# Kernel tuning notes

Measured on AMD Instinct MI355X. Metric: run time of the kernel, lower is better.

Reference implementation:

```python
import jax, jax.numpy as jnp
import numpy as np

B, T, D_MODEL = 2, 2048, 2048
H, HD = 16, 128          # num_heads, head_dim
KV_L, Q_L, R = 512, 1024, 64  # kv_latent, q_latent, qk_rope_dim


def apply_rope(x, freqs):
    # x: (..., T, R); freqs: (T, R//2) angles theta (torch stores exp(i*theta))
    # torch pairs consecutive elements: view(..., R//2, 2) as complex
    xr = x.reshape(x.shape[:-1] + (R // 2, 2))
    x0, x1 = xr[..., 0], xr[..., 1]
    cos, sin = jnp.cos(freqs), jnp.sin(freqs)  # broadcast over leading dims
    y0 = x0 * cos - x1 * sin
    y1 = x0 * sin + x1 * cos
    return jnp.stack([y0, y1], axis=-1).reshape(x.shape)


def setup_inputs() -> dict:
    key = jax.random.key(0)
    ks = jax.random.split(key, 10)
    s = 0.02
    return {
        "x": jax.random.normal(ks[0], (B, T, D_MODEL), jnp.float32),
        "freqs": jax.random.normal(ks[1], (T, R // 2), jnp.float32),
        # weights stored as (in, out) so forward is x @ W (== torch x @ W.T)
        "W_DKV": jax.random.normal(ks[2], (D_MODEL, KV_L), jnp.float32) * s,
        "W_UK": jax.random.normal(ks[3], (KV_L, H * HD), jnp.float32) * s,
        "W_UV": jax.random.normal(ks[4], (KV_L, H * HD), jnp.float32) * s,
        "W_KR": jax.random.normal(ks[5], (D_MODEL, R), jnp.float32) * s,
        "W_DQ": jax.random.normal(ks[6], (D_MODEL, Q_L), jnp.float32) * s,
        "W_UQ": jax.random.normal(ks[7], (Q_L, H * HD), jnp.float32) * s,
        "W_QR": jax.random.normal(ks[8], (Q_L, H * R), jnp.float32) * s,
        "W_O": jax.random.normal(ks[9], (H * HD, D_MODEL), jnp.float32) * s,
    }


def reference(x, freqs, W_DKV, W_UK, W_UV, W_KR, W_DQ, W_UQ, W_QR, W_O):
    b, t, _ = x.shape
    # compressed KV latent and expansions
    c_KV = x @ W_DKV                                             # (B,T,KV_L)
    K_c = (c_KV @ W_UK).reshape(b, t, H, HD).transpose(0, 2, 1, 3)  # (B,H,T,HD)
    V = (c_KV @ W_UV).reshape(b, t, H, HD).transpose(0, 2, 1, 3)    # (B,H,T,HD)
    # shared (single-head) rope key
    K_r1 = apply_rope((x @ W_KR)[:, None, :, :], freqs)          # (B,1,T,R)
    K_r = jnp.broadcast_to(K_r1, (b, H, t, R))
    # compressed Q latent
    c_Q = x @ W_DQ                                               # (B,T,Q_L)
    Q_c = (c_Q @ W_UQ).reshape(b, t, H, HD).transpose(0, 2, 1, 3)
    Q_r = apply_rope((c_Q @ W_QR).reshape(b, t, H, R).transpose(0, 2, 1, 3), freqs)
    Q = jnp.concatenate([Q_c, Q_r], axis=-1)                     # (B,H,T,HD+R)
    K = jnp.concatenate([K_c, K_r], axis=-1)
    # causal SDPA, scale = 1/sqrt(HD+R) (torch default: query last dim)
    scale = 1.0 / jnp.sqrt(jnp.asarray(HD + R, Q.dtype))
    scores = jnp.einsum("bhqe,bhke->bhqk", Q, K) * scale
    causal = jnp.tril(jnp.ones((t, t), bool))
    scores = jnp.where(causal, scores, jnp.asarray(-1e30, scores.dtype))
    attn = jax.nn.softmax(scores, axis=-1)
    out = jnp.einsum("bhqk,bhkd->bhqd", attn, V)                 # (B,H,T,HD)
    out = out.transpose(0, 2, 1, 3).reshape(b, t, H * HD)
    y = out @ W_O                                                # (B,T,D_MODEL)
    return (y, c_KV, K_r1[:, 0, :, :])
```

## Files before the change

### kernel.cpp

```cpp
#include <hip/hip_runtime.h>
#include <stdint.h>

typedef unsigned short u16;
typedef __attribute__((ext_vector_type(8))) short s16x8;
typedef __attribute__((ext_vector_type(4))) float f32x4;

#define B_   2
#define T_   2048
#define DM   2048
#define H_   16
#define HD_  128
#define R_   64
#define E_   192
#define SCALE2 0.104117542f

__device__ __forceinline__ u16 f2b(float f) {
  union { float f; uint32_t u; } x; x.f = f;
  uint32_t u = x.u;
  return (u16)((u + 0x7FFFu + ((u >> 16) & 1u)) >> 16);
}
__device__ __forceinline__ float b2f(u16 h) {
  union { uint32_t u; float f; } x; x.u = ((uint32_t)h) << 16;
  return x.f;
}
__device__ __forceinline__ unsigned pk2(float a, float b) {
  union { float f; unsigned u; } A, B; A.f = a; B.f = b;
  return (B.u & 0xFFFF0000u) | (A.u >> 16);
}
__device__ __forceinline__ void ld_lds16(const void* g, void* l) {
  __builtin_amdgcn_global_load_lds((const __attribute__((address_space(1))) void*)g,
                                   (__attribute__((address_space(3))) void*)l,
                                   16, 0, 0);
}

__device__ __forceinline__ void conv_dev(const float* __restrict__ in, u16* __restrict__ out, int i) {
  float4 v = *(const float4*)(in + (size_t)i * 4);
  ushort4 o;
  o.x = f2b(v.x); o.y = f2b(v.y); o.z = f2b(v.z); o.w = f2b(v.w);
  *(ushort4*)(out + (size_t)i * 4) = o;
}
__device__ __forceinline__ void tr64(const float* __restrict__ in, u16* __restrict__ out,
                                     int K, int N, int bx, int by) {
  __shared__ u16 t[64][65];
  int bn = bx * 64, bk = by * 64;
  int tid = threadIdx.x;
  int r0 = tid >> 4, c0 = (tid & 15) * 4;
#pragma unroll
  for (int rr = 0; rr < 64; rr += 16) {
    float4 v = *(const float4*)(in + (size_t)(bk + r0 + rr) * N + bn + c0);
    t[r0 + rr][c0 + 0] = f2b(v.x); t[r0 + rr][c0 + 1] = f2b(v.y);
    t[r0 + rr][c0 + 2] = f2b(v.z); t[r0 + rr][c0 + 3] = f2b(v.w);
  }
  __syncthreads();
#pragma unroll
  for (int rr = 0; rr < 64; rr += 16) {
    ushort4 v;
    v.x = t[c0 + 0][r0 + rr]; v.y = t[c0 + 1][r0 + rr];
    v.z = t[c0 + 2][r0 + rr]; v.w = t[c0 + 3][r0 + rr];
    *(ushort4*)(out + (size_t)(bn + r0 + rr) * K + bk + c0) = v;
  }
}

__global__ __launch_bounds__(256)
void ta_k(const float* __restrict__ x, const float* __restrict__ fr,
          u16* __restrict__ x_bf, u16* __restrict__ fr_bf,
          const float* __restrict__ wdkv, const float* __restrict__ wkr,
          const float* __restrict__ wdq, u16* __restrict__ W) {
  int id = blockIdx.x;
  if (id < 8192)        conv_dev(x, x_bf, id * 256 + threadIdx.x);
  else if (id < 8256)   conv_dev(fr, fr_bf, (id - 8192) * 256 + threadIdx.x);
  else if (id < 8512) { int i = id - 8256; tr64(wdkv, W, 2048, 512, i & 7, i >> 3); }
  else if (id < 8544) { int i = id - 8512; tr64(wkr, W + 512 * 2048, 2048, 64, 0, i); }
  else                { int i = id - 8544; tr64(wdq, W + 576 * 2048, 2048, 1024, i & 15, i >> 4); }
}
__global__ __launch_bounds__(256)
void tb1_k(const float* __restrict__ wuk, const float* __restrict__ wuv, u16* __restrict__ W) {
  int id = blockIdx.x;
  if (id < 256) tr64(wuk, W, 512, 2048, id & 31, id >> 5);
  else { int i = id - 256; tr64(wuv, W + 2048 * 512, 512, 2048, i & 31, i >> 5); }
}
__global__ __launch_bounds__(256)
void tb2_k(const float* __restrict__ wuq, const float* __restrict__ wqr, u16* __restrict__ W) {
  int id = blockIdx.x;
  if (id < 512) tr64(wuq, W, 1024, 2048, id & 31, id >> 5);
  else { int i = id - 512; tr64(wqr, W + 2048 * 1024, 1024, 1024, i & 15, i >> 4); }
}
__global__ __launch_bounds__(256)
void tc_k(const float* __restrict__ wo, u16* __restrict__ W) {
  tr64(wo, W, 2048, 2048, blockIdx.x & 31, blockIdx.x >> 5);
}

template <int EPI>
__global__ __launch_bounds__(256)
void gemm_bf16(const u16* __restrict__ A, const u16* __restrict__ Bt,
               u16* __restrict__ O0, u16* __restrict__ O1, u16* __restrict__ O2,
               float* __restrict__ OF, float* __restrict__ OF2,
               const u16* __restrict__ FR, int M, int N, int K) {
  __shared__ __align__(16) u16 Al[2][128 * 32];
  __shared__ __align__(16) u16 Bl[2][128 * 32];
  const int tid = threadIdx.x;
  const int ln = tid & 63, w = tid >> 6;
  const int quad = ln >> 4, l16 = ln & 15;
  const int wm = (w >> 1) * 64, wn = (w & 1) * 64;
  const int m0 = blockIdx.y * 128, n0 = blockIdx.x * 128;

  f32x4 zz = {0.f, 0.f, 0.f, 0.f};
  f32x4 acc[4][4];
#pragma unroll
  for (int i = 0; i < 4; i++)
#pragma unroll
    for (int j = 0; j < 4; j++) acc[i][j] = zz;

  const u16* aG[2];
  const u16* bG[2];
  int ldsC[2];
#pragma unroll
  for (int r = 0; r < 2; r++) {
    int i = tid + r * 256;
    int row = i >> 2, cq = (i & 3) * 8;
    aG[r] = A + (size_t)(m0 + row) * K + cq;
    int rb = n0 + row;
    if (rb > N - 1) rb = N - 1;
    bG[r] = Bt + (size_t)rb * K + cq;
    ldsC[r] = ((tid & ~63) + r * 256) * 8;
  }

  for (int k = 0; k < K; k += 64) {
#pragma unroll
    for (int hh = 0; hh < 2; hh++)
#pragma unroll
      for (int r = 0; r < 2; r++) {
        ld_lds16(aG[r] + k + hh * 32, &Al[hh][ldsC[r]]);
        ld_lds16(bG[r] + k + hh * 32, &Bl[hh][ldsC[r]]);
      }
    __syncthreads();
#pragma unroll
    for (int hh = 0; hh < 2; hh++) {
      s16x8 af[4], bf[4];
#pragma unroll
      for (int f = 0; f < 4; f++)
        af[f] = *(const s16x8*)&Al[hh][(wm + f * 16 + l16) * 32 + quad * 8];
#pragma unroll
      for (int f = 0; f < 4; f++)
        bf[f] = *(const s16x8*)&Bl[hh][(wn + f * 16 + l16) * 32 + quad * 8];
#pragma unroll
      for (int i = 0; i < 4; i++)
#pragma unroll
        for (int j = 0; j < 4; j++)
          acc[i][j] = __builtin_amdgcn_mfma_f32_16x16x32_bf16(af[i], bf[j], acc[i][j], 0, 0, 0);
    }
    __syncthreads();
  }

#pragma unroll
  for (int fm = 0; fm < 4; fm++) {
#pragma unroll
    for (int fn = 0; fn < 4; fn++) {
      int n = n0 + wn + fn * 16 + l16;
      int mb = m0 + wm + fm * 16 + quad * 4;
      if (EPI == 2) {
        if (n < N) {
#pragma unroll
          for (int rg = 0; rg < 4; rg++) OF[(size_t)(mb + rg) * N + n] = acc[fm][fn][rg];
        }
      } else if (EPI == 4) {
        if (n < 2048) {
#pragma unroll
          for (int rg = 0; rg < 4; rg++) O0[(size_t)(mb + rg) * 2048 + n] = f2b(acc[fm][fn][rg]);
        } else {
          int hd = n - 2048, b = mb >> 11, t = mb & 2047;
          ushort4 v;
          v.x = f2b(acc[fm][fn][0]); v.y = f2b(acc[fm][fn][1]);
          v.z = f2b(acc[fm][fn][2]); v.w = f2b(acc[fm][fn][3]);
          *(ushort4*)(O1 + ((size_t)(b * 2048 + hd) * 2048 + t)) = v;
        }
      } else if (EPI == 5) {
        if (n < 2048) {
#pragma unroll
          for (int rg = 0; rg < 4; rg++) O0[(size_t)(mb + rg) * 2048 + n] = f2b(acc[fm][fn][rg]);
        } else {
#pragma unroll
          for (int rg = 0; rg < 4; rg++) O1[(size_t)(mb + rg) * 1024 + (n - 2048)] = f2b(acc[fm][fn][rg]);
        }
      } else {
        if (n < 512) {
#pragma unroll
          for (int rg = 0; rg < 4; rg++) {
            float v = acc[fm][fn][rg];
            O0[(size_t)(mb + rg) * 512 + n] = f2b(v);
            OF[(size_t)(mb + rg) * 512 + n] = v;
          }
        } else if (n < 576) {
          int r = n - 512, r2 = r >> 1, odd = r & 1;
#pragma unroll
          for (int rg = 0; rg < 4; rg++) {
            float v = acc[fm][fn][rg];
            float p = __shfl_xor(v, 1);
            int t = mb + rg;
            float a = b2f(FR[(size_t)(t & 2047) * 32 + r2]);
            float sn, cs;
            __sincosf(a, &sn, &cs);
            float y = odd ? (p * sn + v * cs) : (v * cs - p * sn);
            O1[(size_t)t * 64 + r] = f2b(y);
            OF2[(size_t)t * 64 + r] = y;
          }
        } else if (n < 1600) {
#pragma unroll
          for (int rg = 0; rg < 4; rg++) O2[(size_t)(mb + rg) * 1024 + (n - 576)] = f2b(acc[fm][fn][rg]);
        }
      }
    }
  }
}

#define KT_S 200
#define VT_S 72
__global__ __launch_bounds__(512, 2)
void flash_attn(const u16* __restrict__ Qc, const u16* __restrict__ Qr,
                const u16* __restrict__ Kc, const u16* __restrict__ Kr,
                const u16* __restrict__ VT, const u16* __restrict__ fr,
                u16* __restrict__ O) {
  __shared__ __align__(16) u16 Kt[64 * KT_S];
  __shared__ __align__(16) u16 Vt[144 * VT_S];

  const int tid = threadIdx.x;
  const int ln = tid & 63, w = tid >> 6;
  const int quad = ln >> 4, l16 = ln & 15;
  const int bh = blockIdx.x, b = bh >> 4, h = bh & 15;

  for (int i = tid; i < 1024; i += 512) Vt[(128 + (i >> 6)) * VT_S + (i & 63)] = 0x3F80;

  const u16* kBase[3]; int kStep[3], kLds[3];
#pragma unroll
  for (int r = 0; r < 3; r++) {
    int i = tid + r * 512;
    int key = i / 24, c = i - key * 24;
    kLds[r] = key * KT_S + c * 8;
    if (c < 16) { kBase[r] = Kc + ((size_t)(b * T_ + key) * DM + h * HD_ + c * 8); kStep[r] = 64 * DM; }
    else        { kBase[r] = Kr + ((size_t)(b * T_ + key) * R_ + (c - 16) * 8);    kStep[r] = 64 * R_; }
  }
  const u16* vBase[2]; int vLds[2];
#pragma unroll
  for (int r = 0; r < 2; r++) {
    int i = tid + r * 512;
    int row = i >> 3, c = i & 7, c2 = c & 3;
    vLds[r] = row * VT_S + (c >> 2) * 32 + ((2 * c2) & 3) * 8 + (c2 >> 1) * 4;
    vBase[r] = VT + ((size_t)(bh * HD_ + row) * T_ + c * 8);
  }

  f32x4 zz = {0.f, 0.f, 0.f, 0.f};
  const int q0 = (15 - (int)blockIdx.y) * 128;
  const int qw = q0 + w * 16;

  s16x8 qf[6];
  {
    int t = qw + l16;
    const u16* p = Qc + ((size_t)(b * T_ + t) * DM + h * HD_ + quad * 8);
#pragma unroll
    for (int f = 0; f < 4; f++) qf[f] = *(const s16x8*)(p + f * 32);
    const u16* pr = Qr + ((size_t)(b * T_ + t) * (H_ * R_) + h * R_ + quad * 8);
#pragma unroll
    for (int half = 0; half < 2; half++) {
      s16x8 v = *(const s16x8*)(pr + half * 32);
      s16x8 o2;
#pragma unroll
      for (int p2 = 0; p2 < 4; p2++) {
        float a = b2f(fr[t * 32 + half * 16 + quad * 4 + p2]);
        float sn, cs;
        __sincosf(a, &sn, &cs);
        float x0 = b2f((u16)v[2 * p2]), x1 = b2f((u16)v[2 * p2 + 1]);
        o2[2 * p2] = (short)f2b(x0 * cs - x1 * sn);
        o2[2 * p2 + 1] = (short)f2b(x0 * sn + x1 * cs);
      }
      qf[4 + half] = o2;
    }
  }

  f32x4 o[9];
#pragma unroll
  for (int f = 0; f < 9; f++) o[f] = zz;
  float mL = -1e30f;

  const u16* pk[3]; const u16* pv[2];
  s16x8 kv[3], vv[2];
#pragma unroll
  for (int r = 0; r < 3; r++) { pk[r] = kBase[r]; kv[r] = *(const s16x8*)pk[r]; }
#pragma unroll
  for (int r = 0; r < 2; r++) { pv[r] = vBase[r]; vv[r] = *(const s16x8*)pv[r]; }

  const int nk = q0 + 128;
  for (int k0 = 0; k0 < nk; k0 += 64) {
    __syncthreads();
#pragma unroll
    for (int r = 0; r < 3; r++) *(s16x8*)&Kt[kLds[r]] = kv[r];
#pragma unroll
    for (int r = 0; r < 2; r++) {
      union { s16x8 v; uint4 u; } V_; V_.v = vv[r];
      uint2 lo; lo.x = V_.u.x; lo.y = V_.u.y;
      uint2 hi; hi.x = V_.u.z; hi.y = V_.u.w;
      *(uint2*)&Vt[vLds[r]] = lo;
      *(uint2*)&Vt[vLds[r] + 8] = hi;
    }
    __syncthreads();
    if (k0 + 64 < nk) {
#pragma unroll
      for (int r = 0; r < 3; r++) { pk[r] += kStep[r]; kv[r] = *(const s16x8*)pk[r]; }
#pragma unroll
      for (int r = 0; r < 2; r++) { pv[r] += 64; vv[r] = *(const s16x8*)pv[r]; }
    }
    if (k0 > qw + 15) continue;

    f32x4 s[4];
#pragma unroll
    for (int kg = 0; kg < 4; kg++) s[kg] = zz;
#pragma unroll
    for (int e = 0; e < 6; e++)
#pragma unroll
      for (int kg = 0; kg < 4; kg++) {
        s16x8 kf = *(const s16x8*)&Kt[(kg * 16 + l16) * KT_S + e * 32 + quad * 8];
        s[kg] = __builtin_amdgcn_mfma_f32_16x16x32_bf16(kf, qf[e], s[kg], 0, 0, 0);
      }
    const int q = qw + l16;
    float sv[16];
    if (k0 + 63 <= qw) {
#pragma unroll
      for (int kg = 0; kg < 4; kg++)
#pragma unroll
        for (int rg = 0; rg < 4; rg++) sv[kg * 4 + rg] = s[kg][rg] * SCALE2;
    } else {
#pragma unroll
      for (int kg = 0; kg < 4; kg++)
#pragma unroll
        for (int rg = 0; rg < 4; rg++) {
          int key = k0 + kg * 16 + quad * 4 + rg;
          sv[kg * 4 + rg] = (key > q) ? -1e30f : s[kg][rg] * SCALE2;
        }
    }
    float mxa = fmaxf(fmaxf(sv[0], sv[1]), fmaxf(sv[2], sv[3]));
    float mxb = fmaxf(fmaxf(sv[4], sv[5]), fmaxf(sv[6], sv[7]));
    float mxc = fmaxf(fmaxf(sv[8], sv[9]), fmaxf(sv[10], sv[11]));
    float mxd = fmaxf(fmaxf(sv[12], sv[13]), fmaxf(sv[14], sv[15]));
    float mx = fmaxf(fmaxf(mxa, mxb), fmaxf(mxc, mxd));
    mx = fmaxf(mx, __shfl_xor(mx, 16));
    mx = fmaxf(mx, __shfl_xor(mx, 32));
    if (__any(mx > mL)) {
      float mn = fmaxf(mL, mx);
      float alpha = exp2f(mL - mn);
      mL = mn;
      float al[4];
#pragma unroll
      for (int rg = 0; rg < 4; rg++) al[rg] = __shfl(alpha, (ln & 48) | (quad * 4 + rg));
#pragma unroll
      for (int f = 0; f < 9; f++)
#pragma unroll
        for (int rg = 0; rg < 4; rg++) o[f][rg] *= al[rg];
    }
    float p[16];
#pragma unroll
    for (int j = 0; j < 16; j++) p[j] = exp2f(sv[j] - mL);
    union { unsigned pw[8]; s16x8 pa[2]; } P_;
#pragma unroll
    for (int kg = 0; kg < 4; kg++) {
      P_.pw[kg * 2 + 0] = pk2(p[kg * 4 + 0], p[kg * 4 + 1]);
      P_.pw[kg * 2 + 1] = pk2(p[kg * 4 + 2], p[kg * 4 + 3]);
    }
#pragma unroll
    for (int f = 0; f < 9; f++) {
      s16x8 vb0 = *(const s16x8*)&Vt[(f * 16 + l16) * VT_S + quad * 8];
      o[f] = __builtin_amdgcn_mfma_f32_16x16x32_bf16(P_.pa[0], vb0, o[f], 0, 0, 0);
      s16x8 vb1 = *(const s16x8*)&Vt[(f * 16 + l16) * VT_S + 32 + quad * 8];
      o[f] = __builtin_amdgcn_mfma_f32_16x16x32_bf16(P_.pa[1], vb1, o[f], 0, 0, 0);
    }
  }

  float inv[4];
#pragma unroll
  for (int rg = 0; rg < 4; rg++) inv[rg] = 1.0f / o[8][rg];
#pragma unroll
  for (int f = 0; f < 8; f++) {
#pragma unroll
    for (int rg = 0; rg < 4; rg++) {
      int qq = qw + quad * 4 + rg;
      O[(size_t)(b * T_ + qq) * DM + h * HD_ + f * 16 + l16] = f2b(o[f][rg] * inv[rg]);
    }
  }
}

extern "C" void kernel_launch(void* const* d_in, const int* in_sizes, int n_in,
                              void* d_out, int out_size, void* d_ws, size_t ws_size,
                              hipStream_t stream) {
  const float* x    = (const float*)d_in[0];
  const float* fr   = (const float*)d_in[1];
  const float* wdkv = (const float*)d_in[2];
  const float* wuk  = (const float*)d_in[3];
  const float* wuv  = (const float*)d_in[4];
  const float* wkr  = (const float*)d_in[5];
  const float* wdq  = (const float*)d_in[6];
  const float* wuq  = (const float*)d_in[7];
  const float* wqr  = (const float*)d_in[8];
  const float* wo   = (const float*)d_in[9];
  u16* ws = (u16*)d_ws;

  const int M1 = 1048576;
  u16* x_bf  = ws;
  u16* Om    = ws;
  u16* Kc    = ws + 8 * M1;
  u16* VTm   = ws + 16 * M1;
  u16* Qc    = ws + 24 * M1;
  u16* Qr    = ws + 32 * M1;
  u16* W     = ws + 36 * M1;
  u16* cKV   = ws + 40 * M1;
  u16* cQ    = ws + 42 * M1;
  u16* fr_bf = ws + 46 * M1;
  u16* kr_bf = fr_bf + 65536;

  float* out_y   = (float*)d_out;
  float* out_ckv = (float*)d_out + 8388608;
  float* out_kr  = (float*)d_out + 10485760;
  (void)in_sizes; (void)n_in; (void)out_size; (void)ws_size;

  dim3 blk(256);

  ta_k<<<dim3(9056), blk, 0, stream>>>(x, fr, x_bf, fr_bf, wdkv, wkr, wdq, W);
  gemm_bf16<6><<<dim3(13, 32), blk, 0, stream>>>(x_bf, W, cKV, kr_bf, cQ, out_ckv, out_kr, fr_bf,
                                                 4096, 1600, 2048);
  tb1_k<<<dim3(512), blk, 0, stream>>>(wuk, wuv, W);
  gemm_bf16<4><<<dim3(32, 32), blk, 0, stream>>>(cKV, W, Kc, VTm, nullptr, nullptr, nullptr, nullptr,
                                                 4096, 4096, 512);
  tb2_k<<<dim3(768), blk, 0, stream>>>(wuq, wqr, W);
  gemm_bf16<5><<<dim3(24, 32), blk, 0, stream>>>(cQ, W, Qc, Qr, nullptr, nullptr, nullptr, nullptr,
                                                 4096, 3072, 1024);
  flash_attn<<<dim3(32, 16), dim3(512), 0, stream>>>(Qc, Qr, Kc, kr_bf, VTm, fr_bf, Om);
  tc_k<<<dim3(1024), blk, 0, stream>>>(wo, W);
  gemm_bf16<2><<<dim3(16, 32), blk, 0, stream>>>(Om, W, nullptr, nullptr, nullptr, out_y, nullptr,
                                                 nullptr, 4096, 2048, 2048);
}
```

Baseline: 392.1 us.

## Merge weight transposes and up-projection GEMMs into fewer launches

When the workspace is large enough, the W_UK/W_UV/W_UQ/W_QR transposes are folded into the first conversion kernel, writing to dedicated workspace regions. The K/V and Q up-projection GEMMs then run as one combined launch that dispatches blocks to either problem by block index. This removes four kernel launches and the serialization gaps between them, and lets the two GEMMs share the GPU at once. It costs extra workspace and enlarges the first kernel; a fallback keeps the old path when the workspace is too small.

```diff
diff --git a/kernel.cpp b/kernel.cpp
--- a/kernel.cpp
+++ b/kernel.cpp
@@ -65,13 +65,20 @@
 void ta_k(const float* __restrict__ x, const float* __restrict__ fr,
           u16* __restrict__ x_bf, u16* __restrict__ fr_bf,
           const float* __restrict__ wdkv, const float* __restrict__ wkr,
-          const float* __restrict__ wdq, u16* __restrict__ W) {
+          const float* __restrict__ wdq, u16* __restrict__ W,
+          const float* __restrict__ wuk, const float* __restrict__ wuv,
+          const float* __restrict__ wuq, const float* __restrict__ wqr,
+          u16* __restrict__ UKUV, u16* __restrict__ UQQR) {
   int id = blockIdx.x;
   if (id < 8192)        conv_dev(x, x_bf, id * 256 + threadIdx.x);
   else if (id < 8256)   conv_dev(fr, fr_bf, (id - 8192) * 256 + threadIdx.x);
   else if (id < 8512) { int i = id - 8256; tr64(wdkv, W, 2048, 512, i & 7, i >> 3); }
   else if (id < 8544) { int i = id - 8512; tr64(wkr, W + 512 * 2048, 2048, 64, 0, i); }
-  else                { int i = id - 8544; tr64(wdq, W + 576 * 2048, 2048, 1024, i & 15, i >> 4); }
+  else if (id < 9056) { int i = id - 8544; tr64(wdq, W + 576 * 2048, 2048, 1024, i & 15, i >> 4); }
+  else if (id < 9312) { int i = id - 9056; tr64(wuk, UKUV, 512, 2048, i & 31, i >> 5); }
+  else if (id < 9568) { int i = id - 9312; tr64(wuv, UKUV + 2048 * 512, 512, 2048, i & 31, i >> 5); }
+  else if (id < 10080){ int i = id - 9568; tr64(wuq, UQQR, 1024, 2048, i & 31, i >> 5); }
+  else                { int i = id - 10080; tr64(wqr, UQQR + 2048 * 1024, 1024, 1024, i & 15, i >> 4); }
 }
 __global__ __launch_bounds__(256)
 void tb1_k(const float* __restrict__ wuk, const float* __restrict__ wuv, u16* __restrict__ W) {
@@ -91,18 +98,16 @@
 }
 
 template <int EPI>
-__global__ __launch_bounds__(256)
-void gemm_bf16(const u16* __restrict__ A, const u16* __restrict__ Bt,
+__device__ __forceinline__ void gemm_body(u16* Al, u16* Bl,
+               const u16* __restrict__ A, const u16* __restrict__ Bt,
                u16* __restrict__ O0, u16* __restrict__ O1, u16* __restrict__ O2,
                float* __restrict__ OF, float* __restrict__ OF2,
-               const u16* __restrict__ FR, int M, int N, int K) {
-  __shared__ __align__(16) u16 Al[2][128 * 32];
-  __shared__ __align__(16) u16 Bl[2][128 * 32];
+               const u16* __restrict__ FR, int M, int N, int K, int bx, int by) {
   const int tid = threadIdx.x;
   const int ln = tid & 63, w = tid >> 6;
   const int quad = ln >> 4, l16 = ln & 15;
   const int wm = (w >> 1) * 64, wn = (w & 1) * 64;
-  const int m0 = blockIdx.y * 128, n0 = blockIdx.x * 128;
+  const int m0 = by * 128, n0 = bx * 128;
 
   f32x4 zz = {0.f, 0.f, 0.f, 0.f};
   f32x4 acc[4][4];
@@ -130,8 +135,8 @@
     for (int hh = 0; hh < 2; hh++)
 #pragma unroll
       for (int r = 0; r < 2; r++) {
-        ld_lds16(aG[r] + k + hh * 32, &Al[hh][ldsC[r]]);
-        ld_lds16(bG[r] + k + hh * 32, &Bl[hh][ldsC[r]]);
+        ld_lds16(aG[r] + k + hh * 32, &Al[hh * 4096 + ldsC[r]]);
+        ld_lds16(bG[r] + k + hh * 32, &Bl[hh * 4096 + ldsC[r]]);
       }
     __syncthreads();
 #pragma unroll
@@ -139,10 +144,10 @@
       s16x8 af[4], bf[4];
 #pragma unroll
       for (int f = 0; f < 4; f++)
-        af[f] = *(const s16x8*)&Al[hh][(wm + f * 16 + l16) * 32 + quad * 8];
+        af[f] = *(const s16x8*)&Al[hh * 4096 + (wm + f * 16 + l16) * 32 + quad * 8];
 #pragma unroll
       for (int f = 0; f < 4; f++)
-        bf[f] = *(const s16x8*)&Bl[hh][(wn + f * 16 + l16) * 32 + quad * 8];
+        bf[f] = *(const s16x8*)&Bl[hh * 4096 + (wn + f * 16 + l16) * 32 + quad * 8];
 #pragma unroll
       for (int i = 0; i < 4; i++)
 #pragma unroll
@@ -210,6 +215,35 @@
         }
       }
     }
+  }
+}
+
+template <int EPI>
+__global__ __launch_bounds__(256)
+void gemm_bf16(const u16* __restrict__ A, const u16* __restrict__ Bt,
+               u16* __restrict__ O0, u16* __restrict__ O1, u16* __restrict__ O2,
+               float* __restrict__ OF, float* __restrict__ OF2,
+               const u16* __restrict__ FR, int M, int N, int K) {
+  __shared__ __align__(16) u16 Al[2 * 128 * 32];
+  __shared__ __align__(16) u16 Bl[2 * 128 * 32];
+  gemm_body<EPI>(Al, Bl, A, Bt, O0, O1, O2, OF, OF2, FR, M, N, K, blockIdx.x, blockIdx.y);
+}
+
+__global__ __launch_bounds__(256)
+void kvq_k(const u16* __restrict__ cKV, const u16* __restrict__ UKUV,
+           u16* __restrict__ Kc, u16* __restrict__ VT,
+           const u16* __restrict__ cQ, const u16* __restrict__ UQQR,
+           u16* __restrict__ Qc, u16* __restrict__ Qr) {
+  __shared__ __align__(16) u16 Al[2 * 128 * 32];
+  __shared__ __align__(16) u16 Bl[2 * 128 * 32];
+  int id = blockIdx.x;
+  if (id < 768) {
+    gemm_body<5>(Al, Bl, cQ, UQQR, Qc, Qr, nullptr, nullptr, nullptr, nullptr,
+                 4096, 3072, 1024, id % 24, id / 24);
+  } else {
+    int j = id - 768;
+    gemm_body<4>(Al, Bl, cKV, UKUV, Kc, VT, nullptr, nullptr, nullptr, nullptr,
+                 4096, 4096, 512, j & 31, j >> 5);
   }
 }
 
@@ -401,7 +435,7 @@
   const float* wo   = (const float*)d_in[9];
   u16* ws = (u16*)d_ws;
 
-  const int M1 = 1048576;
+  const size_t M1 = 1048576;
   u16* x_bf  = ws;
   u16* Om    = ws;
   u16* Kc    = ws + 8 * M1;
@@ -413,23 +447,35 @@
   u16* cQ    = ws + 42 * M1;
   u16* fr_bf = ws + 46 * M1;
   u16* kr_bf = fr_bf + 65536;
+  u16* UKUV  = ws + 47 * M1;
+  u16* UQQR  = ws + 49 * M1;
 
   float* out_y   = (float*)d_out;
   float* out_ckv = (float*)d_out + 8388608;
   float* out_kr  = (float*)d_out + 10485760;
-  (void)in_sizes; (void)n_in; (void)out_size; (void)ws_size;
+  (void)in_sizes; (void)n_in; (void)out_size;
 
   dim3 blk(256);
-
-  ta_k<<<dim3(9056), blk, 0, stream>>>(x, fr, x_bf, fr_bf, wdkv, wkr, wdq, W);
-  gemm_bf16<6><<<dim3(13, 32), blk, 0, stream>>>(x_bf, W, cKV, kr_bf, cQ, out_ckv, out_kr, fr_bf,
-                                                 4096, 1600, 2048);
-  tb1_k<<<dim3(512), blk, 0, stream>>>(wuk, wuv, W);
-  gemm_bf16<4><<<dim3(32, 32), blk, 0, stream>>>(cKV, W, Kc, VTm, nullptr, nullptr, nullptr, nullptr,
-                                                 4096, 4096, 512);
-  tb2_k<<<dim3(768), blk, 0, stream>>>(wuq, wqr, W);
-  gemm_bf16<5><<<dim3(24, 32), blk, 0, stream>>>(cQ, W, Qc, Qr, nullptr, nullptr, nullptr, nullptr,
-                                                 4096, 3072, 1024);
+  const bool merged = ws_size >= (size_t)52 * M1 * 2;
+
+  if (merged) {
+    ta_k<<<dim3(10336), blk, 0, stream>>>(x, fr, x_bf, fr_bf, wdkv, wkr, wdq, W,
+                                          wuk, wuv, wuq, wqr, UKUV, UQQR);
+    gemm_bf16<6><<<dim3(13, 32), blk, 0, stream>>>(x_bf, W, cKV, kr_bf, cQ, out_ckv, out_kr, fr_bf,
+                                                   4096, 1600, 2048);
+    kvq_k<<<dim3(1792), blk, 0, stream>>>(cKV, UKUV, Kc, VTm, cQ, UQQR, Qc, Qr);
+  } else {
+    ta_k<<<dim3(9056), blk, 0, stream>>>(x, fr, x_bf, fr_bf, wdkv, wkr, wdq, W,
+                                         wuk, wuv, wuq, wqr, UKUV, UQQR);
+    gemm_bf16<6><<<dim3(13, 32), blk, 0, stream>>>(x_bf, W, cKV, kr_bf, cQ, out_ckv, out_kr, fr_bf,
+                                                   4096, 1600, 2048);
+    tb1_k<<<dim3(512), blk, 0, stream>>>(wuk, wuv, W);
+    gemm_bf16<4><<<dim3(32, 32), blk, 0, stream>>>(cKV, W, Kc, VTm, nullptr, nullptr, nullptr,
+                                                   nullptr, 4096, 4096, 512);
+    tb2_k<<<dim3(768), blk, 0, stream>>>(wuq, wqr, W);
+    gemm_bf16<5><<<dim3(24, 32), blk, 0, stream>>>(cQ, W, Qc, Qr, nullptr, nullptr, nullptr,
+                                                   nullptr, 4096, 3072, 1024);
+  }
   flash_attn<<<dim3(32, 16), dim3(512), 0, stream>>>(Qc, Qr, Kc, kr_bf, VTm, fr_bf, Om);
   tc_k<<<dim3(1024), blk, 0, stream>>>(wo, W);
   gemm_bf16<2><<<dim3(16, 32), blk, 0, stream>>>(Om, W, nullptr, nullptr, nullptr, out_y, nullptr,
```

New measurement: 378.6 us. 1.04x faster.
